# Optimization experiments

Measured on AMD Instinct MI355X. Metric: run time of the kernel, lower is better.

The kernel has to match this reference:

```python
import jax, jax.numpy as jnp
import numpy as np
from jax import lax

D_MODEL = 1024
D_STATE = 64
D_CONV = 4
EXPAND = 2
HEADDIM = 64
D_INNER = EXPAND * D_MODEL            # 2048
NHEADS = D_INNER // HEADDIM           # 32
NGROUPS = 1
CONV_DIM = D_INNER + 2 * NGROUPS * D_STATE   # 2176
D_IN_PROJ = 2 * D_INNER + 2 * NGROUPS * D_STATE + NHEADS  # 4256
BATCH, SEQLEN = 2, 4096
EPS = 1e-5


def setup_inputs() -> dict:
    key = jax.random.key(0)
    ks = jax.random.split(key, 8)
    x = jax.random.normal(ks[0], (BATCH, SEQLEN, D_MODEL), jnp.float32)
    ln_w = jnp.ones((D_MODEL,), jnp.float32)
    ln_b = jnp.zeros((D_MODEL,), jnp.float32)
    W_in = jax.random.normal(ks[1], (D_IN_PROJ, D_MODEL), jnp.float32) * (D_MODEL ** -0.5)
    conv_w = jax.random.normal(ks[2], (CONV_DIM, D_CONV), jnp.float32) * (D_CONV ** -0.5)
    conv_b = jnp.zeros((CONV_DIM,), jnp.float32)
    # dt init as in mamba2: softplus^{-1} of dt in [1e-3, 1e-1]
    dt = jax.random.uniform(ks[3], (NHEADS,), jnp.float32, 1e-3, 1e-1)
    dt_bias = jnp.log(jnp.expm1(dt))
    A_log = jnp.log(jax.random.uniform(ks[4], (NHEADS,), jnp.float32, 1.0, 16.0))
    D = jnp.ones((NHEADS,), jnp.float32)
    norm_w = jnp.ones((D_INNER,), jnp.float32)
    W_out = jax.random.normal(ks[5], (D_MODEL, D_INNER), jnp.float32) * (D_INNER ** -0.5)
    return {"x": x, "ln_w": ln_w, "ln_b": ln_b, "W_in": W_in, "conv_w": conv_w,
            "conv_b": conv_b, "dt_bias": dt_bias, "A_log": A_log, "D": D,
            "norm_w": norm_w, "W_out": W_out}


def _mamba2_forward(x, ln_w, ln_b, W_in, conv_w, conv_b, dt_bias, A_log, D, norm_w, W_out):
    B, L, _ = x.shape
    # pre-norm (LayerNorm)
    mu = jnp.mean(x, -1, keepdims=True)
    var = jnp.mean(jnp.square(x - mu), -1, keepdims=True)
    u = (x - mu) * lax.rsqrt(var + EPS) * ln_w + ln_b
    # in_proj
    zxbcdt = jnp.einsum('bld,ed->ble', u, W_in)        # [B,L,D_IN_PROJ]
    z = zxbcdt[..., :D_INNER]                          # gate
    xBC = zxbcdt[..., D_INNER:D_INNER + CONV_DIM]
    dt = zxbcdt[..., D_INNER + CONV_DIM:]              # [B,L,H]
    # causal depthwise conv1d + silu
    lhs = jnp.transpose(xBC, (0, 2, 1))                # [B,C,L]
    rhs = conv_w[:, None, :]                           # [C,1,K]
    conv = lax.conv_general_dilated(lhs, rhs, (1,), [(D_CONV - 1, 0)],
                                    dimension_numbers=('NCH', 'OIH', 'NCH'),
                                    feature_group_count=CONV_DIM)
    xBC = jax.nn.silu(jnp.transpose(conv, (0, 2, 1)) + conv_b)  # [B,L,C]
    xs = xBC[..., :D_INNER].reshape(B, L, NHEADS, HEADDIM)      # [B,L,H,P]
    Bm = xBC[..., D_INNER:D_INNER + D_STATE]                    # [B,L,N]
    Cm = xBC[..., D_INNER + D_STATE:]                           # [B,L,N]
    dt = jax.nn.softplus(dt + dt_bias)                          # [B,L,H]
    A = -jnp.exp(A_log)                                         # [H]
    # selective scan over time
    def step(h, inp):
        dt_t, x_t, B_t, C_t = inp          # [B,H],[B,H,P],[B,N],[B,N]
        dA = jnp.exp(dt_t * A)             # [B,H]
        dBx = (dt_t[..., None] * x_t)[..., None] * B_t[:, None, None, :]
        h = h * dA[..., None, None] + dBx  # [B,H,P,N]
        y = jnp.einsum('bhpn,bn->bhp', h, C_t)
        return h, y

    h0 = jnp.zeros((B, NHEADS, HEADDIM, D_STATE), x.dtype)
    xs_t = (jnp.transpose(dt, (1, 0, 2)), jnp.transpose(xs, (1, 0, 2, 3)),
            jnp.transpose(Bm, (1, 0, 2)), jnp.transpose(Cm, (1, 0, 2)))
    _, ys = lax.scan(step, h0, xs_t)                   # [L,B,H,P]
    y = jnp.transpose(ys, (1, 0, 2, 3)) + D[None, None, :, None] * xs
    y = y.reshape(B, L, D_INNER)
    # gated RMSNorm (norm_before_gate=False): rmsnorm(y * silu(z)) * w
    y = y * jax.nn.silu(z)
    y = y * lax.rsqrt(jnp.mean(jnp.square(y), -1, keepdims=True) + EPS) * norm_w
    out = jnp.einsum('ble,de->bld', y, W_out)
    # residual; dropout is identity in eval
    return x + out


def reference(x, ln_w, ln_b, W_in, conv_w, conv_b, dt_bias, A_log, D, norm_w, W_out):
    return _mamba2_forward(x, ln_w, ln_b, W_in, conv_w, conv_b, dt_bias, A_log, D, norm_w, W_out)
```

## Files before the change

kernel.cpp:

```cpp
#include <hip/hip_runtime.h>
#include <math.h>

typedef unsigned short u16;
typedef __attribute__((ext_vector_type(4))) float f32x4;
typedef __attribute__((ext_vector_type(8))) short s16x8;
typedef __attribute__((ext_vector_type(8))) unsigned short u16x8;
typedef __attribute__((ext_vector_type(4))) unsigned short u16x4;

__device__ __forceinline__ float bf2f(u16 v) {
    union { unsigned u; float f; } c; c.u = ((unsigned)v) << 16; return c.f;
}
__device__ __forceinline__ u16 f2bf(float f) {
    union { float f; unsigned u; } c; c.f = f;
    unsigned x = c.u;
    unsigned r = (x + 0x7fffu + ((x >> 16) & 1u)) >> 16;
    return (u16)r;
}

__device__ __forceinline__ void async_copy16(const u16* g, u16* l) {
    __builtin_amdgcn_global_load_lds(
        (const __attribute__((address_space(1))) unsigned int*)g,
        (__attribute__((address_space(3))) unsigned int*)l, 16, 0, 0);
}

__global__ __launch_bounds__(256)
void cvt_kernel(const float* __restrict__ in, u16* __restrict__ out, int n4) {
    int i = blockIdx.x * 256 + threadIdx.x;
    if (i >= n4) return;
    float4 v = reinterpret_cast<const float4*>(in)[i];
    u16x4 o;
    o[0] = f2bf(v.x); o[1] = f2bf(v.y); o[2] = f2bf(v.z); o[3] = f2bf(v.w);
    reinterpret_cast<u16x4*>(out)[i] = o;
}

__global__ __launch_bounds__(256)
void ln_kernel(const float* __restrict__ x, const float* __restrict__ w,
               const float* __restrict__ b, u16* __restrict__ u) {
    int row = blockIdx.x, t = threadIdx.x;
    const float* xr = x + (size_t)row * 1024;
    float4 xv = *reinterpret_cast<const float4*>(xr + t * 4);
    float f[4] = {xv.x, xv.y, xv.z, xv.w};
    float s = 0.f, sq = 0.f;
    #pragma unroll
    for (int i = 0; i < 4; i++) { s += f[i]; sq += f[i] * f[i]; }
    #pragma unroll
    for (int o = 32; o; o >>= 1) { s += __shfl_down(s, o); sq += __shfl_down(sq, o); }
    __shared__ float rs[4], rq[4];
    int lane = t & 63, wv = t >> 6;
    if (!lane) { rs[wv] = s; rq[wv] = sq; }
    __syncthreads();
    s = rs[0] + rs[1] + rs[2] + rs[3];
    sq = rq[0] + rq[1] + rq[2] + rq[3];
    float mu = s * (1.f / 1024.f);
    float var = sq * (1.f / 1024.f) - mu * mu;
    float rstd = rsqrtf(var + 1e-5f);
    float4 wv4 = *reinterpret_cast<const float4*>(w + t * 4);
    float4 bv4 = *reinterpret_cast<const float4*>(b + t * 4);
    float wf[4] = {wv4.x, wv4.y, wv4.z, wv4.w};
    float bf[4] = {bv4.x, bv4.y, bv4.z, bv4.w};
    u16x4 o4;
    #pragma unroll
    for (int i = 0; i < 4; i++)
        o4[i] = f2bf((f[i] - mu) * rstd * wf[i] + bf[i]);
    *reinterpret_cast<u16x4*>(u + (size_t)row * 1024 + t * 4) = o4;
}

__global__ __launch_bounds__(256)
void gemm_in_kernel(const u16* __restrict__ A, const u16* __restrict__ W,
                    u16* __restrict__ zbuf, u16* __restrict__ xbc,
                    float* __restrict__ dtsp, const float* __restrict__ dt_bias,
                    int M, int N, int K) {
    __shared__ __align__(16) u16 As[128 * 32];
    __shared__ __align__(16) u16 Bs[128 * 32];
    int t = threadIdx.x;
    int m0 = blockIdx.x * 128, n0 = blockIdx.y * 128;
    int wave = t >> 6, lane = t & 63;
    int wm = (wave >> 1) * 64, wn = (wave & 1) * 64;
    int lm = lane & 15, lq = lane >> 4;
    int srow = lane >> 2, scol = (lane & 3) * 8;
    f32x4 acc[4][4];
    #pragma unroll
    for (int i = 0; i < 4; i++)
        #pragma unroll
        for (int j = 0; j < 4; j++) acc[i][j] = (f32x4){0.f, 0.f, 0.f, 0.f};

    for (int k0 = 0; k0 < K; k0 += 32) {
        #pragma unroll
        for (int s = 0; s < 2; s++) {
            int ch = s * 4 + wave;
            int row = ch * 16 + srow;
            async_copy16(A + (size_t)(m0 + row) * K + k0 + scol, &As[ch * 512 + lane * 8]);
            int rn = n0 + row;
            if (rn < N)
                async_copy16(W + (size_t)rn * K + k0 + scol, &Bs[ch * 512 + lane * 8]);
        }
        __syncthreads();
        s16x8 af[4], bfr[4];
        #pragma unroll
        for (int i = 0; i < 4; i++)
            af[i] = *reinterpret_cast<const s16x8*>(&As[(wm + i * 16 + lm) * 32 + lq * 8]);
        #pragma unroll
        for (int j = 0; j < 4; j++)
            bfr[j] = *reinterpret_cast<const s16x8*>(&Bs[(wn + j * 16 + lm) * 32 + lq * 8]);
        #pragma unroll
        for (int i = 0; i < 4; i++)
            #pragma unroll
            for (int j = 0; j < 4; j++)
                acc[i][j] = __builtin_amdgcn_mfma_f32_16x16x32_bf16(af[i], bfr[j], acc[i][j], 0, 0, 0);
        __syncthreads();
    }
    #pragma unroll
    for (int i = 0; i < 4; i++) {
        #pragma unroll
        for (int j = 0; j < 4; j++) {
            int col = n0 + wn + j * 16 + lm;
            if (col < N) {
                #pragma unroll
                for (int r = 0; r < 4; r++) {
                    int row = m0 + wm + i * 16 + lq * 4 + r;
                    float v = acc[i][j][r];
                    if (col < 2048) {
                        zbuf[(size_t)row * 2048 + col] = f2bf(v);
                    } else if (col < 4224) {
                        xbc[(size_t)row * 2176 + (col - 2048)] = f2bf(v);
                    } else {
                        float tt = v + dt_bias[col - 4224];
                        float sp = (tt > 20.f) ? tt : log1pf(expf(tt));
                        dtsp[(size_t)row * 32 + (col - 4224)] = sp;
                    }
                }
            }
        }
    }
}

__global__ __launch_bounds__(256)
void gemm_out_kernel(const u16* __restrict__ A, const u16* __restrict__ W,
                     float* __restrict__ C, const float* __restrict__ resid,
                     int M, int N, int K) {
    __shared__ __align__(16) u16 As[128 * 32];
    __shared__ __align__(16) u16 Bs[128 * 32];
    int t = threadIdx.x;
    int m0 = blockIdx.x * 128, n0 = blockIdx.y * 128;
    int wave = t >> 6, lane = t & 63;
    int wm = (wave >> 1) * 64, wn = (wave & 1) * 64;
    int lm = lane & 15, lq = lane >> 4;
    int srow = lane >> 2, scol = (lane & 3) * 8;
    f32x4 acc[4][4];
    #pragma unroll
    for (int i = 0; i < 4; i++)
        #pragma unroll
        for (int j = 0; j < 4; j++) acc[i][j] = (f32x4){0.f, 0.f, 0.f, 0.f};
    for (int k0 = 0; k0 < K; k0 += 32) {
        #pragma unroll
        for (int s = 0; s < 2; s++) {
            int ch = s * 4 + wave;
            int row = ch * 16 + srow;
            async_copy16(A + (size_t)(m0 + row) * K + k0 + scol, &As[ch * 512 + lane * 8]);
            async_copy16(W + (size_t)(n0 + row) * K + k0 + scol, &Bs[ch * 512 + lane * 8]);
        }
        __syncthreads();
        s16x8 af[4], bfr[4];
        #pragma unroll
        for (int i = 0; i < 4; i++)
            af[i] = *reinterpret_cast<const s16x8*>(&As[(wm + i * 16 + lm) * 32 + lq * 8]);
        #pragma unroll
        for (int j = 0; j < 4; j++)
            bfr[j] = *reinterpret_cast<const s16x8*>(&Bs[(wn + j * 16 + lm) * 32 + lq * 8]);
        #pragma unroll
        for (int i = 0; i < 4; i++)
            #pragma unroll
            for (int j = 0; j < 4; j++)
                acc[i][j] = __builtin_amdgcn_mfma_f32_16x16x32_bf16(af[i], bfr[j], acc[i][j], 0, 0, 0);
        __syncthreads();
    }
    #pragma unroll
    for (int i = 0; i < 4; i++)
        #pragma unroll
        for (int j = 0; j < 4; j++) {
            int col = n0 + wn + j * 16 + lm;
            #pragma unroll
            for (int r = 0; r < 4; r++) {
                int row = m0 + wm + i * 16 + lq * 4 + r;
                size_t off = (size_t)row * N + col;
                C[off] = acc[i][j][r] + resid[off];
            }
        }
}

__global__ __launch_bounds__(256)
void conv_kernel(const u16* __restrict__ xbc, const float* __restrict__ cw,
                 const float* __restrict__ cb, u16* __restrict__ xact) {
    int idx = blockIdx.x * 256 + threadIdx.x;
    if (idx >= 8192 * 2176) return;
    int c = idx % 2176;
    int bl = idx / 2176;
    int l = bl & 4095, b = bl >> 12;
    float acc = cb[c];
    #pragma unroll
    for (int k = 0; k < 4; k++) {
        int lk = l - 3 + k;
        if (lk >= 0)
            acc += cw[c * 4 + k] * bf2f(xbc[(size_t)(b * 4096 + lk) * 2176 + c]);
    }
    float s = acc / (1.f + expf(-acc));
    xact[(size_t)bl * 2176 + c] = f2bf(s);
}

#define TS 72
__device__ __forceinline__ void mfma_quad(const u16* Pa, const u16* Qb,
                                          int mh, int nh, int lm, int lq,
                                          f32x4 acc[2][2]) {
    #pragma unroll
    for (int ks = 0; ks < 2; ks++) {
        s16x8 a[2], b[2];
        #pragma unroll
        for (int ti = 0; ti < 2; ti++)
            a[ti] = *reinterpret_cast<const s16x8*>(&Pa[(mh * 32 + ti * 16 + lm) * TS + ks * 32 + lq * 8]);
        #pragma unroll
        for (int tj = 0; tj < 2; tj++)
            b[tj] = *reinterpret_cast<const s16x8*>(&Qb[(nh * 32 + tj * 16 + lm) * TS + ks * 32 + lq * 8]);
        #pragma unroll
        for (int ti = 0; ti < 2; ti++)
            #pragma unroll
            for (int tj = 0; tj < 2; tj++)
                acc[ti][tj] = __builtin_amdgcn_mfma_f32_16x16x32_bf16(a[ti], b[tj], acc[ti][tj], 0, 0, 0);
    }
}

__global__ __launch_bounds__(256)
void chunk_dh_kernel(const u16* __restrict__ xact, const float* __restrict__ dtsp,
                     const float* __restrict__ A_log,
                     float* __restrict__ ssum, u16* __restrict__ dH) {
    int blk = blockIdx.x;
    int c = blk & 63, h = (blk >> 6) & 31, b = blk >> 11;
    __shared__ __align__(16) u16 Xw[64 * TS];
    __shared__ __align__(16) u16 Bt[64 * TS];
    __shared__ float sW[64];
    int t = threadIdx.x;
    int row0 = b * 4096 + c * 64;
    if (t < 64) {
        float dtv = dtsp[(size_t)(row0 + t) * 32 + h];
        float Ah = -__expf(A_log[h]);
        float s = dtv * Ah;
        #pragma unroll
        for (int o = 1; o < 64; o <<= 1) {
            float up = __shfl_up(s, o);
            if (t >= o) s += up;
        }
        float slast = __shfl(s, 63);
        sW[t] = __expf(slast - s) * dtv;
        ssum[(size_t)blk * 64 + t] = s;
    }
    __syncthreads();
    int j = t & 63, cg = (t >> 6) * 16;
    {
        float wj = sW[j];
        const u16* xr = xact + (size_t)(row0 + j) * 2176 + h * 64 + cg;
        u16x8 v0 = *reinterpret_cast<const u16x8*>(xr);
        u16x8 v1 = *reinterpret_cast<const u16x8*>(xr + 8);
        #pragma unroll
        for (int i = 0; i < 8; i++) Xw[(cg + i) * TS + j] = f2bf(bf2f(v0[i]) * wj);
        #pragma unroll
        for (int i = 0; i < 8; i++) Xw[(cg + 8 + i) * TS + j] = f2bf(bf2f(v1[i]) * wj);
        const u16* br = xact + (size_t)(row0 + j) * 2176 + 2048 + cg;
        u16x8 w0 = *reinterpret_cast<const u16x8*>(br);
        u16x8 w1 = *reinterpret_cast<const u16x8*>(br + 8);
        #pragma unroll
        for (int i = 0; i < 8; i++) Bt[(cg + i) * TS + j] = w0[i];
        #pragma unroll
        for (int i = 0; i < 8; i++) Bt[(cg + 8 + i) * TS + j] = w1[i];
    }
    __syncthreads();
    int wave = t >> 6, lane = t & 63, lm = lane & 15, lq = lane >> 4;
    int mh = wave >> 1, nh = wave & 1;
    f32x4 acc[2][2];
    #pragma unroll
    for (int i = 0; i < 2; i++)
        #pragma unroll
        for (int jj = 0; jj < 2; jj++) acc[i][jj] = (f32x4){0.f, 0.f, 0.f, 0.f};
    mfma_quad(Xw, Bt, mh, nh, lm, lq, acc);
    u16* out = dH + (size_t)blk * 4096;
    #pragma unroll
    for (int ti = 0; ti < 2; ti++)
        #pragma unroll
        for (int tj = 0; tj < 2; tj++)
            #pragma unroll
            for (int r = 0; r < 4; r++) {
                int p = mh * 32 + ti * 16 + lq * 4 + r;
                int n = nh * 32 + tj * 16 + lm;
                out[p * 64 + n] = f2bf(acc[ti][tj][r]);
            }
}

__global__ __launch_bounds__(128)
void chunk_scan_kernel(const u16* __restrict__ dH, const float* __restrict__ ssum,
                       u16* __restrict__ Hst) {
    int bh = blockIdx.x, g = blockIdx.y, t = threadIdx.x;
    int idx = g * 512 + t * 4;
    float H[4] = {0.f, 0.f, 0.f, 0.f};
    for (int c = 0; c < 64; c++) {
        size_t base = ((size_t)bh * 64 + c) * 4096 + idx;
        float lam = __expf(ssum[((size_t)bh * 64 + c) * 64 + 63]);
        u16x4 dh = *reinterpret_cast<const u16x4*>(dH + base);
        u16x4 hv;
        #pragma unroll
        for (int i = 0; i < 4; i++) hv[i] = f2bf(H[i]);
        *reinterpret_cast<u16x4*>(Hst + base) = hv;
        #pragma unroll
        for (int i = 0; i < 4; i++) H[i] = H[i] * lam + bf2f(dh[i]);
    }
}

__global__ __launch_bounds__(256)
void chunk_out_kernel(const u16* __restrict__ xact, const float* __restrict__ dtsp,
                      const float* __restrict__ ssum, const u16* __restrict__ Hst,
                      const float* __restrict__ Dp, u16* __restrict__ yraw) {
    int blk = blockIdx.x;
    int c = blk & 63, h = (blk >> 6) & 31, b = blk >> 11;
    __shared__ __align__(16) u16 Ct[64 * TS];
    __shared__ __align__(16) u16 BM[64 * TS];
    __shared__ __align__(16) u16 Xt[64 * TS];
    __shared__ __align__(16) u16 Hs[64 * TS];
    __shared__ float sS[64], sDt[64], sE[64];
    int t = threadIdx.x;
    int row0 = b * 4096 + c * 64;
    if (t < 64) {
        float dtv = dtsp[(size_t)(row0 + t) * 32 + h];
        float s = ssum[(size_t)blk * 64 + t];
        sS[t] = s; sDt[t] = dtv; sE[t] = __expf(s);
    }
    int r2 = t >> 2, cg2 = (t & 3) * 16;
    {
        const u16* cr = xact + (size_t)(row0 + r2) * 2176 + 2112 + cg2;
        *reinterpret_cast<u16x8*>(&Ct[r2 * TS + cg2]) = *reinterpret_cast<const u16x8*>(cr);
        *reinterpret_cast<u16x8*>(&Ct[r2 * TS + cg2 + 8]) = *reinterpret_cast<const u16x8*>(cr + 8);
        const u16* br = xact + (size_t)(row0 + r2) * 2176 + 2048 + cg2;
        *reinterpret_cast<u16x8*>(&BM[r2 * TS + cg2]) = *reinterpret_cast<const u16x8*>(br);
        *reinterpret_cast<u16x8*>(&BM[r2 * TS + cg2 + 8]) = *reinterpret_cast<const u16x8*>(br + 8);
        const u16* hr = Hst + (size_t)blk * 4096 + r2 * 64 + cg2;
        *reinterpret_cast<u16x8*>(&Hs[r2 * TS + cg2]) = *reinterpret_cast<const u16x8*>(hr);
        *reinterpret_cast<u16x8*>(&Hs[r2 * TS + cg2 + 8]) = *reinterpret_cast<const u16x8*>(hr + 8);
    }
    int j = t & 63, cg = (t >> 6) * 16;
    {
        const u16* xr = xact + (size_t)(row0 + j) * 2176 + h * 64 + cg;
        u16x8 v0 = *reinterpret_cast<const u16x8*>(xr);
        u16x8 v1 = *reinterpret_cast<const u16x8*>(xr + 8);
        #pragma unroll
        for (int i = 0; i < 8; i++) Xt[(cg + i) * TS + j] = v0[i];
        #pragma unroll
        for (int i = 0; i < 8; i++) Xt[(cg + 8 + i) * TS + j] = v1[i];
    }
    __syncthreads();
    int wave = t >> 6, lane = t & 63, lm = lane & 15, lq = lane >> 4;
    int mh = wave >> 1, nh = wave & 1;
    f32x4 g1[2][2], y2[2][2], y3[2][2];
    #pragma unroll
    for (int i = 0; i < 2; i++)
        #pragma unroll
        for (int jj = 0; jj < 2; jj++) {
            g1[i][jj] = (f32x4){0.f, 0.f, 0.f, 0.f};
            y2[i][jj] = (f32x4){0.f, 0.f, 0.f, 0.f};
            y3[i][jj] = (f32x4){0.f, 0.f, 0.f, 0.f};
        }
    mfma_quad(Ct, BM, mh, nh, lm, lq, g1);
    __syncthreads();
    #pragma unroll
    for (int ti = 0; ti < 2; ti++)
        #pragma unroll
        for (int tj = 0; tj < 2; tj++) {
            int j_ = nh * 32 + tj * 16 + lm;
            float sj = sS[j_], dtj = sDt[j_];
            #pragma unroll
            for (int r = 0; r < 4; r++) {
                int ii = mh * 32 + ti * 16 + lq * 4 + r;
                float v = g1[ti][tj][r] * __expf(sS[ii] - sj) * dtj;
                v = (j_ <= ii) ? v : 0.f;
                BM[ii * TS + j_] = f2bf(v);
            }
        }
    __syncthreads();
    mfma_quad(BM, Xt, mh, nh, lm, lq, y2);
    mfma_quad(Ct, Hs, mh, nh, lm, lq, y3);
    float Dh = Dp[h];
    #pragma unroll
    for (int ti = 0; ti < 2; ti++)
        #pragma unroll
        for (int tj = 0; tj < 2; tj++)
            #pragma unroll
            for (int r = 0; r < 4; r++) {
                int ii = mh * 32 + ti * 16 + lq * 4 + r;
                int p = nh * 32 + tj * 16 + lm;
                float xv = bf2f(Xt[p * TS + ii]);
                float y = y2[ti][tj][r] + sE[ii] * y3[ti][tj][r] + Dh * xv;
                yraw[(size_t)(row0 + ii) * 2048 + h * 64 + p] = f2bf(y);
            }
}

__global__ __launch_bounds__(256)
void gate_kernel(const u16* __restrict__ yraw, const u16* __restrict__ zbuf,
                 const float* __restrict__ nw, u16* __restrict__ yfin) {
    int row = blockIdx.x, t = threadIdx.x;
    u16x8 yv = *reinterpret_cast<const u16x8*>(yraw + (size_t)row * 2048 + t * 8);
    u16x8 zv = *reinterpret_cast<const u16x8*>(zbuf + (size_t)row * 2048 + t * 8);
    float g[8]; float sq = 0.f;
    #pragma unroll
    for (int i = 0; i < 8; i++) {
        float z = bf2f(zv[i]);
        float gg = bf2f(yv[i]) * (z / (1.f + expf(-z)));
        g[i] = gg; sq += gg * gg;
    }
    #pragma unroll
    for (int o = 32; o; o >>= 1) sq += __shfl_down(sq, o);
    __shared__ float rq[4];
    int lane = t & 63, wv = t >> 6;
    if (!lane) rq[wv] = sq;
    __syncthreads();
    sq = rq[0] + rq[1] + rq[2] + rq[3];
    float scale = rsqrtf(sq * (1.f / 2048.f) + 1e-5f);
    float4 n0 = *reinterpret_cast<const float4*>(nw + t * 8);
    float4 n1 = *reinterpret_cast<const float4*>(nw + t * 8 + 4);
    float nf[8] = {n0.x, n0.y, n0.z, n0.w, n1.x, n1.y, n1.z, n1.w};
    u16x8 o8;
    #pragma unroll
    for (int i = 0; i < 8; i++) o8[i] = f2bf(g[i] * scale * nf[i]);
    *reinterpret_cast<u16x8*>(yfin + (size_t)row * 2048 + t * 8) = o8;
}

extern "C" void kernel_launch(void* const* d_in, const int* in_sizes, int n_in,
                              void* d_out, int out_size, void* d_ws, size_t ws_size,
                              hipStream_t stream) {
    const float* x       = (const float*)d_in[0];
    const float* ln_w    = (const float*)d_in[1];
    const float* ln_b    = (const float*)d_in[2];
    const float* W_in    = (const float*)d_in[3];
    const float* conv_w  = (const float*)d_in[4];
    const float* conv_b  = (const float*)d_in[5];
    const float* dt_bias = (const float*)d_in[6];
    const float* A_log   = (const float*)d_in[7];
    const float* Dp      = (const float*)d_in[8];
    const float* norm_w  = (const float*)d_in[9];
    const float* W_out   = (const float*)d_in[10];
    float* out = (float*)d_out;

    char* ws = (char*)d_ws;
    u16*  zbuf    = (u16*)(ws + 0);
    u16*  xbc     = (u16*)(ws + 33554432);
    u16*  Hst     = (u16*)(ws + 33554432);
    u16*  xact    = (u16*)(ws + 69206016);
    u16*  yfin    = xact;
    u16*  u_buf   = (u16*)(ws + 104857600);
    float* ssum   = (float*)(ws + 104857600);
    float* dtsp   = (float*)(ws + 121634816);
    u16*  dH      = (u16*)(ws + 122683392);
    u16*  yraw    = (u16*)(ws + 122683392);
    u16*  w_in_bf = (u16*)(ws + 156237824);
    u16*  w_out_bf= (u16*)(ws + 164954112);

    cvt_kernel<<<(1089536 + 255) / 256, 256, 0, stream>>>(W_in, w_in_bf, 1089536);
    cvt_kernel<<<(524288 + 255) / 256, 256, 0, stream>>>(W_out, w_out_bf, 524288);

    ln_kernel<<<8192, 256, 0, stream>>>(x, ln_w, ln_b, u_buf);

    dim3 g1(64, 34);
    gemm_in_kernel<<<g1, 256, 0, stream>>>(u_buf, w_in_bf, zbuf, xbc, dtsp, dt_bias,
                                           8192, 4256, 1024);

    conv_kernel<<<(8192 * 2176) / 256, 256, 0, stream>>>(xbc, conv_w, conv_b, xact);

    chunk_dh_kernel<<<4096, 256, 0, stream>>>(xact, dtsp, A_log, ssum, dH);
    chunk_scan_kernel<<<dim3(64, 8), 128, 0, stream>>>(dH, ssum, Hst);
    chunk_out_kernel<<<4096, 256, 0, stream>>>(xact, dtsp, ssum, Hst, Dp, yraw);

    gate_kernel<<<8192, 256, 0, stream>>>(yraw, zbuf, norm_w, yfin);

    dim3 g2(64, 8);
    gemm_out_kernel<<<g2, 256, 0, stream>>>(yfin, w_out_bf, out, x, 8192, 1024, 2048);
}
```

Measured before the change: 447.8 us.

## Widen GEMM K-step, vectorize conv kernel, merge weight conversion launches

```diff
diff --git a/kernel.cpp b/kernel.cpp
--- a/kernel.cpp
+++ b/kernel.cpp
@@ -24,13 +24,17 @@
 }
 
 __global__ __launch_bounds__(256)
-void cvt_kernel(const float* __restrict__ in, u16* __restrict__ out, int n4) {
+void cvt_kernel(const float* __restrict__ in_a, u16* __restrict__ out_a, int n4a,
+                const float* __restrict__ in_b, u16* __restrict__ out_b, int n4b) {
     int i = blockIdx.x * 256 + threadIdx.x;
-    if (i >= n4) return;
-    float4 v = reinterpret_cast<const float4*>(in)[i];
+    const float* in; u16* out; int k;
+    if (i < n4a) { in = in_a; out = out_a; k = i; }
+    else if (i < n4a + n4b) { in = in_b; out = out_b; k = i - n4a; }
+    else return;
+    float4 v = reinterpret_cast<const float4*>(in)[k];
     u16x4 o;
     o[0] = f2bf(v.x); o[1] = f2bf(v.y); o[2] = f2bf(v.z); o[3] = f2bf(v.w);
-    reinterpret_cast<u16x4*>(out)[i] = o;
+    reinterpret_cast<u16x4*>(out)[k] = o;
 }
 
 __global__ __launch_bounds__(256)
@@ -70,8 +74,8 @@
                     u16* __restrict__ zbuf, u16* __restrict__ xbc,
                     float* __restrict__ dtsp, const float* __restrict__ dt_bias,
                     int M, int N, int K) {
-    __shared__ __align__(16) u16 As[128 * 32];
-    __shared__ __align__(16) u16 Bs[128 * 32];
+    __shared__ __align__(16) u16 As[2 * 128 * 32];
+    __shared__ __align__(16) u16 Bs[2 * 128 * 32];
     int t = threadIdx.x;
     int m0 = blockIdx.x * 128, n0 = blockIdx.y * 128;
     int wave = t >> 6, lane = t & 63;
@@ -84,29 +88,37 @@
         #pragma unroll
         for (int j = 0; j < 4; j++) acc[i][j] = (f32x4){0.f, 0.f, 0.f, 0.f};
 
-    for (int k0 = 0; k0 < K; k0 += 32) {
-        #pragma unroll
-        for (int s = 0; s < 2; s++) {
-            int ch = s * 4 + wave;
-            int row = ch * 16 + srow;
-            async_copy16(A + (size_t)(m0 + row) * K + k0 + scol, &As[ch * 512 + lane * 8]);
-            int rn = n0 + row;
-            if (rn < N)
-                async_copy16(W + (size_t)rn * K + k0 + scol, &Bs[ch * 512 + lane * 8]);
+    for (int k0 = 0; k0 < K; k0 += 64) {
+        #pragma unroll
+        for (int p = 0; p < 2; p++) {
+            #pragma unroll
+            for (int s = 0; s < 2; s++) {
+                int ch = s * 4 + wave;
+                int row = ch * 16 + srow;
+                async_copy16(A + (size_t)(m0 + row) * K + k0 + p * 32 + scol,
+                             &As[p * 4096 + ch * 512 + lane * 8]);
+                int rn = n0 + row;
+                if (rn < N)
+                    async_copy16(W + (size_t)rn * K + k0 + p * 32 + scol,
+                                 &Bs[p * 4096 + ch * 512 + lane * 8]);
+            }
         }
         __syncthreads();
-        s16x8 af[4], bfr[4];
-        #pragma unroll
-        for (int i = 0; i < 4; i++)
-            af[i] = *reinterpret_cast<const s16x8*>(&As[(wm + i * 16 + lm) * 32 + lq * 8]);
-        #pragma unroll
-        for (int j = 0; j < 4; j++)
-            bfr[j] = *reinterpret_cast<const s16x8*>(&Bs[(wn + j * 16 + lm) * 32 + lq * 8]);
-        #pragma unroll
-        for (int i = 0; i < 4; i++)
+        #pragma unroll
+        for (int p = 0; p < 2; p++) {
+            s16x8 af[4], bfr[4];
+            #pragma unroll
+            for (int i = 0; i < 4; i++)
+                af[i] = *reinterpret_cast<const s16x8*>(&As[p * 4096 + (wm + i * 16 + lm) * 32 + lq * 8]);
             #pragma unroll
             for (int j = 0; j < 4; j++)
-                acc[i][j] = __builtin_amdgcn_mfma_f32_16x16x32_bf16(af[i], bfr[j], acc[i][j], 0, 0, 0);
+                bfr[j] = *reinterpret_cast<const s16x8*>(&Bs[p * 4096 + (wn + j * 16 + lm) * 32 + lq * 8]);
+            #pragma unroll
+            for (int i = 0; i < 4; i++)
+                #pragma unroll
+                for (int j = 0; j < 4; j++)
+                    acc[i][j] = __builtin_amdgcn_mfma_f32_16x16x32_bf16(af[i], bfr[j], acc[i][j], 0, 0, 0);
+        }
         __syncthreads();
     }
     #pragma unroll
@@ -138,8 +150,8 @@
 void gemm_out_kernel(const u16* __restrict__ A, const u16* __restrict__ W,
                      float* __restrict__ C, const float* __restrict__ resid,
                      int M, int N, int K) {
-    __shared__ __align__(16) u16 As[128 * 32];
-    __shared__ __align__(16) u16 Bs[128 * 32];
+    __shared__ __align__(16) u16 As[2 * 128 * 32];
+    __shared__ __align__(16) u16 Bs[2 * 128 * 32];
     int t = threadIdx.x;
     int m0 = blockIdx.x * 128, n0 = blockIdx.y * 128;
     int wave = t >> 6, lane = t & 63;
@@ -151,27 +163,35 @@
     for (int i = 0; i < 4; i++)
         #pragma unroll
         for (int j = 0; j < 4; j++) acc[i][j] = (f32x4){0.f, 0.f, 0.f, 0.f};
-    for (int k0 = 0; k0 < K; k0 += 32) {
-        #pragma unroll
-        for (int s = 0; s < 2; s++) {
-            int ch = s * 4 + wave;
-            int row = ch * 16 + srow;
-            async_copy16(A + (size_t)(m0 + row) * K + k0 + scol, &As[ch * 512 + lane * 8]);
-            async_copy16(W + (size_t)(n0 + row) * K + k0 + scol, &Bs[ch * 512 + lane * 8]);
+    for (int k0 = 0; k0 < K; k0 += 64) {
+        #pragma unroll
+        for (int p = 0; p < 2; p++) {
+            #pragma unroll
+            for (int s = 0; s < 2; s++) {
+                int ch = s * 4 + wave;
+                int row = ch * 16 + srow;
+                async_copy16(A + (size_t)(m0 + row) * K + k0 + p * 32 + scol,
+                             &As[p * 4096 + ch * 512 + lane * 8]);
+                async_copy16(W + (size_t)(n0 + row) * K + k0 + p * 32 + scol,
+                             &Bs[p * 4096 + ch * 512 + lane * 8]);
+            }
         }
         __syncthreads();
-        s16x8 af[4], bfr[4];
-        #pragma unroll
-        for (int i = 0; i < 4; i++)
-            af[i] = *reinterpret_cast<const s16x8*>(&As[(wm + i * 16 + lm) * 32 + lq * 8]);
-        #pragma unroll
-        for (int j = 0; j < 4; j++)
-            bfr[j] = *reinterpret_cast<const s16x8*>(&Bs[(wn + j * 16 + lm) * 32 + lq * 8]);
-        #pragma unroll
-        for (int i = 0; i < 4; i++)
+        #pragma unroll
+        for (int p = 0; p < 2; p++) {
+            s16x8 af[4], bfr[4];
+            #pragma unroll
+            for (int i = 0; i < 4; i++)
+                af[i] = *reinterpret_cast<const s16x8*>(&As[p * 4096 + (wm + i * 16 + lm) * 32 + lq * 8]);
             #pragma unroll
             for (int j = 0; j < 4; j++)
-                acc[i][j] = __builtin_amdgcn_mfma_f32_16x16x32_bf16(af[i], bfr[j], acc[i][j], 0, 0, 0);
+                bfr[j] = *reinterpret_cast<const s16x8*>(&Bs[p * 4096 + (wn + j * 16 + lm) * 32 + lq * 8]);
+            #pragma unroll
+            for (int i = 0; i < 4; i++)
+                #pragma unroll
+                for (int j = 0; j < 4; j++)
+                    acc[i][j] = __builtin_amdgcn_mfma_f32_16x16x32_bf16(af[i], bfr[j], acc[i][j], 0, 0, 0);
+        }
         __syncthreads();
     }
     #pragma unroll
@@ -192,19 +212,31 @@
 void conv_kernel(const u16* __restrict__ xbc, const float* __restrict__ cw,
                  const float* __restrict__ cb, u16* __restrict__ xact) {
     int idx = blockIdx.x * 256 + threadIdx.x;
-    if (idx >= 8192 * 2176) return;
-    int c = idx % 2176;
-    int bl = idx / 2176;
+    if (idx >= 8192 * 272) return;
+    int c0 = (idx % 272) * 8;
+    int bl = idx / 272;
     int l = bl & 4095, b = bl >> 12;
-    float acc = cb[c];
+    float acc[8];
+    #pragma unroll
+    for (int i = 0; i < 8; i++) acc[i] = cb[c0 + i];
     #pragma unroll
     for (int k = 0; k < 4; k++) {
         int lk = l - 3 + k;
-        if (lk >= 0)
-            acc += cw[c * 4 + k] * bf2f(xbc[(size_t)(b * 4096 + lk) * 2176 + c]);
-    }
-    float s = acc / (1.f + expf(-acc));
-    xact[(size_t)bl * 2176 + c] = f2bf(s);
+        if (lk >= 0) {
+            u16x8 v = *reinterpret_cast<const u16x8*>(
+                xbc + (size_t)(b * 4096 + lk) * 2176 + c0);
+            #pragma unroll
+            for (int i = 0; i < 8; i++)
+                acc[i] += cw[(c0 + i) * 4 + k] * bf2f(v[i]);
+        }
+    }
+    u16x8 o;
+    #pragma unroll
+    for (int i = 0; i < 8; i++) {
+        float s = acc[i] / (1.f + expf(-acc[i]));
+        o[i] = f2bf(s);
+    }
+    *reinterpret_cast<u16x8*>(xact + (size_t)bl * 2176 + c0) = o;
 }
 
 #define TS 72
@@ -458,8 +490,8 @@
     u16*  w_in_bf = (u16*)(ws + 156237824);
     u16*  w_out_bf= (u16*)(ws + 164954112);
 
-    cvt_kernel<<<(1089536 + 255) / 256, 256, 0, stream>>>(W_in, w_in_bf, 1089536);
-    cvt_kernel<<<(524288 + 255) / 256, 256, 0, stream>>>(W_out, w_out_bf, 524288);
+    cvt_kernel<<<(1089536 + 524288 + 255) / 256, 256, 0, stream>>>(
+        W_in, w_in_bf, 1089536, W_out, w_out_bf, 524288);
 
     ln_kernel<<<8192, 256, 0, stream>>>(x, ln_w, ln_b, u_buf);
 
@@ -467,7 +499,7 @@
     gemm_in_kernel<<<g1, 256, 0, stream>>>(u_buf, w_in_bf, zbuf, xbc, dtsp, dt_bias,
                                            8192, 4256, 1024);
 
-    conv_kernel<<<(8192 * 2176) / 256, 256, 0, stream>>>(xbc, conv_w, conv_b, xact);
+    conv_kernel<<<(8192 * 272) / 256, 256, 0, stream>>>(xbc, conv_w, conv_b, xact);
 
     chunk_dh_kernel<<<4096, 256, 0, stream>>>(xact, dtsp, A_log, ssum, dH);
     chunk_scan_kernel<<<dim3(64, 8), 128, 0, stream>>>(dH, ssum, Hst);
```

Result: slower. 483.5 us (+8.0%).
